# Kernel tuning notes

Measured on AMD Instinct MI355X. Metric: run time of the kernel, lower is better.

## Reference

```python
import jax, jax.numpy as jnp
import numpy as np

N_REC = 3
TEMP = 1.0
BAL_W = 0.01
Z_W = 0.001


def setup_inputs() -> dict:
    key = jax.random.key(0)
    kx, kw = jax.random.split(key)
    x = jax.random.normal(kx, (4, 4096, 2048), dtype=jnp.float32)
    W = 0.02 * jax.random.normal(kw, (N_REC, 2048), dtype=jnp.float32)  # nn.Linear(d_model, n_rec, bias=False), std=0.02
    return {"x": x, "W": W, "recursion_idx": 0}


def _compact(mask, cur_gate, max_k):
    """Vectorized version of the per-batch nonzero/pad loop.
    mask: [B,T] bool, cur_gate: [B,T] float. Returns sel [B,max_k], gv [B,max_k]."""
    counts = jnp.sum(mask, axis=-1)  # [B]
    # stable argsort pushes active (key=0) positions to the front, in order
    key = jnp.where(mask, 0, 1).astype(jnp.int32)
    order = jnp.argsort(key, axis=-1, stable=True)  # [B,T]
    # position j clamps to last valid index (replicates pad-with-last behavior)
    pos = jnp.minimum(jnp.arange(max_k)[None, :], jnp.maximum(counts - 1, 0)[:, None])
    sel = jnp.take_along_axis(order, pos, axis=1)  # [B,max_k]
    empty = (counts == 0)[:, None]
    sel = jnp.where(empty, 0, sel)
    gv = jnp.take_along_axis(cur_gate, sel, axis=1)
    gv = jnp.where(empty, jnp.float32(0.0), gv)
    return sel, gv


def reference(x, W, recursion_idx):
    # router linear + softmax + argmax (one-shot token-choice assignment)
    logits = jnp.einsum('btd,nd->btn', x / TEMP, W)  # [B,T,N_REC]
    gates = jax.nn.softmax(logits, axis=-1)
    assign = jnp.argmax(gates, axis=-1)  # [B,T]
    active_mask = assign >= recursion_idx
    cur_gate = gates[:, :, min(recursion_idx, N_REC - 1)]  # [B,T]
    # max_k is data-dependent (eager, outside jit)
    max_k = max(1, int(jnp.max(jnp.sum(active_mask, axis=-1))))
    sel, gv = _compact(active_mask, cur_gate, max_k)
    selected = sel[..., None]          # [B,max_k,1] int
    gate_weights = gv[..., None]       # [B,max_k,1]
    # training-mode losses (recursion_idx == 0 path)
    fracs = jnp.mean(jax.nn.one_hot(assign, N_REC, dtype=jnp.float32), axis=(0, 1))
    aux_loss = BAL_W * jnp.sum((fracs - 1.0 / N_REC) ** 2)
    z = jax.scipy.special.logsumexp(logits, axis=-1)
    z_loss = Z_W * jnp.mean(z ** 2)
    return selected, gate_weights, logits[:, :, :1], aux_loss, z_loss
```

## Files before the change

kernel.cpp:

```cpp
#include <hip/hip_runtime.h>
#include <hip/hip_bf16.h>

#define B_    4
#define T_    4096
#define D_    2048
#define NTOK  (B_ * T_)
#define NREC  3
#define BAL_W 0.01f
#define Z_W   0.001f
#define NBLK  1024

typedef __attribute__((ext_vector_type(4))) float float4v;

__global__ __launch_bounds__(256) void tcr_f32_phaseA(
    const float* __restrict__ x,
    const float* __restrict__ w,
    const int* __restrict__ ridx_p,
    float* __restrict__ out_f,
    float4v* __restrict__ partials)
{
    const int ridx = ridx_p[0];
    const int jc   = ridx < (NREC - 1) ? (ridx < 0 ? 0 : ridx) : (NREC - 1);
    const int lane = threadIdx.x & 63;
    const int wv   = threadIdx.x >> 6;
    const int wid  = (blockIdx.x * blockDim.x + threadIdx.x) >> 6;
    const int nw   = (gridDim.x * blockDim.x) >> 6;

    float wr[NREC][8][4];
#pragma unroll
    for (int n = 0; n < NREC; ++n)
#pragma unroll
        for (int j = 0; j < 8; ++j) {
            const float4v v = *reinterpret_cast<const float4v*>(w + n * D_ + (j * 64 + lane) * 4);
#pragma unroll
            for (int e = 0; e < 4; ++e) wr[n][j][e] = v[e];
        }

    float z2 = 0.f, c0 = 0.f, c1 = 0.f, c2 = 0.f;

    for (int t = wid; t < NTOK; t += nw) {
        const float* xp = x + (size_t)t * D_;
        float a0 = 0.f, a1 = 0.f, a2 = 0.f;
#pragma unroll
        for (int j = 0; j < 8; ++j) {
            const float4v v = *reinterpret_cast<const float4v*>(xp + (j * 64 + lane) * 4);
#pragma unroll
            for (int e = 0; e < 4; ++e) {
                a0 = fmaf(v[e], wr[0][j][e], a0);
                a1 = fmaf(v[e], wr[1][j][e], a1);
                a2 = fmaf(v[e], wr[2][j][e], a2);
            }
        }
#pragma unroll
        for (int off = 32; off > 0; off >>= 1) {
            a0 += __shfl_xor(a0, off);
            a1 += __shfl_xor(a1, off);
            a2 += __shfl_xor(a2, off);
        }
        if (lane == 0) {
            const float m  = fmaxf(a0, fmaxf(a1, a2));
            const float e0 = expf(a0 - m), e1 = expf(a1 - m), e2 = expf(a2 - m);
            const float s  = e0 + e1 + e2;
            const float z  = m + logf(s);
            int   assign = 0; float best = a0;
            if (a1 > best) { best = a1; assign = 1; }
            if (a2 > best) { best = a2; assign = 2; }
            const float g = (jc == 0 ? e0 : (jc == 1 ? e1 : e2)) / s;

            out_f[NTOK + t]     = (assign >= ridx) ? g : -g;
            out_f[2 * NTOK + t] = a0;

            z2 += z * z;
            if (assign == 0) c0 += 1.f; else if (assign == 1) c1 += 1.f; else c2 += 1.f;
        }
    }

    __shared__ float4v s_part[4];
    if (lane == 0) {
        float4v p; p[0] = z2; p[1] = c0; p[2] = c1; p[3] = c2;
        s_part[wv] = p;
    }
    __syncthreads();
    if (threadIdx.x == 0) {
        float4v p = s_part[0];
#pragma unroll
        for (int i = 1; i < 4; ++i) {
            const float4v q = s_part[i];
#pragma unroll
            for (int e = 0; e < 4; ++e) p[e] += q[e];
        }
        partials[blockIdx.x] = p;
    }
}

__global__ __launch_bounds__(1024) void tcr_f32_phaseB(
    const float4v* __restrict__ partials,
    float* __restrict__ out_f)
{
    __shared__ int      s_sum[1024];
    __shared__ unsigned s_sel[T_];
    __shared__ float    s_g[T_];
    __shared__ float4v  s_red[1024];
    const int b    = blockIdx.x;
    const int tid  = threadIdx.x;
    const int base = b * T_;

    float g[4]; int f[4]; int loc = 0;
#pragma unroll
    for (int r = 0; r < 4; ++r) {
        g[r] = out_f[NTOK + base + tid * 4 + r];
        f[r] = (g[r] > 0.f) ? 1 : 0;
        loc += f[r];
    }
    s_sum[tid] = loc;
    __syncthreads();
    for (int off = 1; off < 1024; off <<= 1) {
        const int v = (tid >= off) ? s_sum[tid - off] : 0;
        __syncthreads();
        s_sum[tid] += v;
        __syncthreads();
    }
    const int cnt = s_sum[1023];
    int pos = s_sum[tid] - loc;
#pragma unroll
    for (int r = 0; r < 4; ++r) {
        if (f[r] && (unsigned)pos < (unsigned)T_) {
            s_sel[pos] = (unsigned)(tid * 4 + r);
            s_g[pos]   = g[r];
            ++pos;
        }
    }
    __syncthreads();

#pragma unroll
    for (int r = 0; r < 4; ++r) {
        const int k = tid + r * 1024;
        float selv, gv;
        if (cnt == 0) { selv = 0.f; gv = 0.f; }
        else {
            const int kk = (k < cnt) ? k : (cnt - 1);
            selv = (float)s_sel[kk];
            gv   = s_g[kk];
        }
        out_f[base + k]        = selv;
        out_f[NTOK + base + k] = gv;
    }

    if (b == 0) {
        s_red[tid] = partials[tid];
        __syncthreads();
        for (int off = 512; off > 0; off >>= 1) {
            if (tid < off) {
                float4v a = s_red[tid], c = s_red[tid + off];
#pragma unroll
                for (int e = 0; e < 4; ++e) a[e] += c[e];
                s_red[tid] = a;
            }
            __syncthreads();
        }
        if (tid == 0) {
            const float4v p = s_red[0];
            const float inv = 1.0f / (float)NTOK;
            float aux = 0.f;
#pragma unroll
            for (int n = 0; n < NREC; ++n) {
                const float d = p[1 + n] * inv - (1.0f / 3.0f);
                aux = fmaf(d, d, aux);
            }
            out_f[3 * NTOK + 0] = BAL_W * aux;
            out_f[3 * NTOK + 1] = Z_W * p[0] * inv;
        }
    }
}

extern "C" void kernel_launch(void* const* d_in, const int* in_sizes, int n_in,
                              void* d_out, int out_size, void* d_ws, size_t ws_size,
                              hipStream_t stream) {
    const float* x  = (const float*)d_in[0];
    const float* w  = (const float*)d_in[1];
    const int* ridx = (const int*)d_in[2];
    float* out_f = (float*)d_out;
    float4v* partials = (float4v*)d_ws;

    tcr_f32_phaseA<<<dim3(NBLK), dim3(256), 0, stream>>>(x, w, ridx, out_f, partials);
    tcr_f32_phaseB<<<dim3(B_), dim3(1024), 0, stream>>>(partials, out_f);
}
```

Baseline: 32.88 us.

## Stage router weights in LDS, batch x loads, use wave-shuffle scans in phase B

Phase A no longer keeps the router weights in 96 registers per lane. It copies them into 24 KB of shared memory per block, doubles the block size to 512 threads, and issues all eight x vector loads before the FMAs so more memory requests are in flight. Phase B replaces the shared-memory Hillis-Steele scan and tree reduction with wave shuffle scans and reductions, which cuts the number of block barriers. The cost is LDS reads of the weights for every token and LDS pressure from the staging buffer.

```diff
diff --git a/kernel.cpp b/kernel.cpp
--- a/kernel.cpp
+++ b/kernel.cpp
@@ -8,47 +8,56 @@
 #define NREC  3
 #define BAL_W 0.01f
 #define Z_W   0.001f
-#define NBLK  1024
+#define ABLK  1024
+#define ATHR  512
 
 typedef __attribute__((ext_vector_type(4))) float float4v;
 
-__global__ __launch_bounds__(256) void tcr_f32_phaseA(
+__global__ __launch_bounds__(ATHR) void tcr7_phaseA(
     const float* __restrict__ x,
     const float* __restrict__ w,
     const int* __restrict__ ridx_p,
     float* __restrict__ out_f,
     float4v* __restrict__ partials)
 {
+    __shared__ float s_w[NREC * D_];
+    {
+        const float4v* src = reinterpret_cast<const float4v*>(w);
+        float4v*       dst = reinterpret_cast<float4v*>(s_w);
+#pragma unroll
+        for (int i = 0; i < (NREC * D_ / 4) / ATHR; ++i)
+            dst[i * ATHR + threadIdx.x] = src[i * ATHR + threadIdx.x];
+    }
+    __syncthreads();
+
     const int ridx = ridx_p[0];
     const int jc   = ridx < (NREC - 1) ? (ridx < 0 ? 0 : ridx) : (NREC - 1);
     const int lane = threadIdx.x & 63;
     const int wv   = threadIdx.x >> 6;
-    const int wid  = (blockIdx.x * blockDim.x + threadIdx.x) >> 6;
-    const int nw   = (gridDim.x * blockDim.x) >> 6;
-
-    float wr[NREC][8][4];
-#pragma unroll
-    for (int n = 0; n < NREC; ++n)
-#pragma unroll
-        for (int j = 0; j < 8; ++j) {
-            const float4v v = *reinterpret_cast<const float4v*>(w + n * D_ + (j * 64 + lane) * 4);
-#pragma unroll
-            for (int e = 0; e < 4; ++e) wr[n][j][e] = v[e];
-        }
+    const int wid  = (blockIdx.x * ATHR + threadIdx.x) >> 6;
+    const int nw   = (gridDim.x * ATHR) >> 6;
 
     float z2 = 0.f, c0 = 0.f, c1 = 0.f, c2 = 0.f;
 
     for (int t = wid; t < NTOK; t += nw) {
         const float* xp = x + (size_t)t * D_;
+        float4v xv[8];
+#pragma unroll
+        for (int j = 0; j < 8; ++j)
+            xv[j] = *reinterpret_cast<const float4v*>(xp + (j * 64 + lane) * 4);
+
         float a0 = 0.f, a1 = 0.f, a2 = 0.f;
 #pragma unroll
         for (int j = 0; j < 8; ++j) {
-            const float4v v = *reinterpret_cast<const float4v*>(xp + (j * 64 + lane) * 4);
+            const int kb = (j * 64 + lane) * 4;
+            const float4v w0 = *reinterpret_cast<const float4v*>(&s_w[kb]);
+            const float4v w1 = *reinterpret_cast<const float4v*>(&s_w[D_ + kb]);
+            const float4v w2 = *reinterpret_cast<const float4v*>(&s_w[2 * D_ + kb]);
 #pragma unroll
             for (int e = 0; e < 4; ++e) {
-                a0 = fmaf(v[e], wr[0][j][e], a0);
-                a1 = fmaf(v[e], wr[1][j][e], a1);
-                a2 = fmaf(v[e], wr[2][j][e], a2);
+                a0 = fmaf(xv[j][e], w0[e], a0);
+                a1 = fmaf(xv[j][e], w1[e], a1);
+                a2 = fmaf(xv[j][e], w2[e], a2);
             }
         }
 #pragma unroll
@@ -75,7 +84,7 @@
         }
     }
 
-    __shared__ float4v s_part[4];
+    __shared__ float4v s_part[ATHR / 64];
     if (lane == 0) {
         float4v p; p[0] = z2; p[1] = c0; p[2] = c1; p[3] = c2;
         s_part[wv] = p;
@@ -84,7 +93,7 @@
     if (threadIdx.x == 0) {
         float4v p = s_part[0];
 #pragma unroll
-        for (int i = 1; i < 4; ++i) {
+        for (int i = 1; i < ATHR / 64; ++i) {
             const float4v q = s_part[i];
 #pragma unroll
             for (int e = 0; e < 4; ++e) p[e] += q[e];
@@ -93,16 +102,18 @@
     }
 }
 
-__global__ __launch_bounds__(1024) void tcr_f32_phaseB(
+__global__ __launch_bounds__(1024) void tcr7_phaseB(
     const float4v* __restrict__ partials,
     float* __restrict__ out_f)
 {
-    __shared__ int      s_sum[1024];
+    __shared__ int      s_ws[16];
     __shared__ unsigned s_sel[T_];
     __shared__ float    s_g[T_];
-    __shared__ float4v  s_red[1024];
+    __shared__ float4v  s_red[16];
     const int b    = blockIdx.x;
     const int tid  = threadIdx.x;
+    const int lane = tid & 63;
+    const int wv   = tid >> 6;
     const int base = b * T_;
 
     float g[4]; int f[4]; int loc = 0;
@@ -112,16 +123,22 @@
         f[r] = (g[r] > 0.f) ? 1 : 0;
         loc += f[r];
     }
-    s_sum[tid] = loc;
-    __syncthreads();
-    for (int off = 1; off < 1024; off <<= 1) {
-        const int v = (tid >= off) ? s_sum[tid - off] : 0;
-        __syncthreads();
-        s_sum[tid] += v;
-        __syncthreads();
-    }
-    const int cnt = s_sum[1023];
-    int pos = s_sum[tid] - loc;
+    int isc = loc;
+#pragma unroll
+    for (int off = 1; off < 64; off <<= 1) {
+        const int u = __shfl_up(isc, off);
+        if (lane >= off) isc += u;
+    }
+    if (lane == 63) s_ws[wv] = isc;
+    __syncthreads();
+    int wbase = 0, cnt = 0;
+#pragma unroll
+    for (int i = 0; i < 16; ++i) {
+        const int v = s_ws[i];
+        cnt += v;
+        if (i < wv) wbase += v;
+    }
+    int pos = wbase + isc - loc;
 #pragma unroll
     for (int r = 0; r < 4; ++r) {
         if (f[r] && (unsigned)pos < (unsigned)T_) {
@@ -146,30 +163,33 @@
         out_f[NTOK + base + k] = gv;
     }
 
-    if (b == 0) {
-        s_red[tid] = partials[tid];
-        __syncthreads();
-        for (int off = 512; off > 0; off >>= 1) {
-            if (tid < off) {
-                float4v a = s_red[tid], c = s_red[tid + off];
-#pragma unroll
-                for (int e = 0; e < 4; ++e) a[e] += c[e];
-                s_red[tid] = a;
-            }
-            __syncthreads();
-        }
-        if (tid == 0) {
-            const float4v p = s_red[0];
-            const float inv = 1.0f / (float)NTOK;
-            float aux = 0.f;
-#pragma unroll
-            for (int n = 0; n < NREC; ++n) {
-                const float d = p[1 + n] * inv - (1.0f / 3.0f);
-                aux = fmaf(d, d, aux);
-            }
-            out_f[3 * NTOK + 0] = BAL_W * aux;
-            out_f[3 * NTOK + 1] = Z_W * p[0] * inv;
-        }
+    float4v p;
+    if (b == 0) p = partials[tid];
+    else { p[0] = 0.f; p[1] = 0.f; p[2] = 0.f; p[3] = 0.f; }
+#pragma unroll
+    for (int off = 32; off > 0; off >>= 1) {
+#pragma unroll
+        for (int e = 0; e < 4; ++e) p[e] += __shfl_xor(p[e], off);
+    }
+    if (lane == 0) s_red[wv] = p;
+    __syncthreads();
+    if (b == 0 && tid == 0) {
+        float4v q = s_red[0];
+#pragma unroll
+        for (int i = 1; i < 16; ++i) {
+            const float4v r2 = s_red[i];
+#pragma unroll
+            for (int e = 0; e < 4; ++e) q[e] += r2[e];
+        }
+        const float inv = 1.0f / (float)NTOK;
+        float aux = 0.f;
+#pragma unroll
+        for (int n = 0; n < NREC; ++n) {
+            const float d = q[1 + n] * inv - (1.0f / 3.0f);
+            aux = fmaf(d, d, aux);
+        }
+        out_f[3 * NTOK + 0] = BAL_W * aux;
+        out_f[3 * NTOK + 1] = Z_W * q[0] * inv;
     }
 }
 
@@ -182,6 +202,6 @@
     float* out_f = (float*)d_out;
     float4v* partials = (float4v*)d_ws;
 
-    tcr_f32_phaseA<<<dim3(NBLK), dim3(256), 0, stream>>>(x, w, ridx, out_f, partials);
-    tcr_f32_phaseB<<<dim3(B_), dim3(1024), 0, stream>>>(partials, out_f);
+    tcr7_phaseA<<<dim3(ABLK), dim3(ATHR), 0, stream>>>(x, w, ridx, out_f, partials);
+    tcr7_phaseB<<<dim3(B_), dim3(1024), 0, stream>>>(partials, out_f);
 }
```

Result: slower. 33.63 us (+2.3%).
